# Kernel optimization log

Measured on AMD Instinct MI355X. Metric: run time of the kernel, lower is better.

## Reference

```python
import jax, jax.numpy as jnp
import numpy as np

N, E, H, D, F_IN = 50000, 400000, 2, 128, 5
EPS = 1e-5  # BatchNorm eps

def _bn(x, gamma, beta, rm, rv):
    # eval-mode BatchNorm1d using running stats
    return (x - rm) * jax.lax.rsqrt(rv + EPS) * gamma + beta

def setup_inputs() -> dict:
    key = jax.random.key(0)
    ks = jax.random.split(key, 24)
    r = lambda i, shape, s=1.0: jax.random.normal(ks[i], shape, jnp.float32) * s
    u = lambda i, shape: jax.random.uniform(ks[i], shape, jnp.float32)
    return {
        "h": r(0, (N, F_IN)),
        "edge_index": jax.random.randint(ks[1], (2, E), 0, N),
        "edge_weight": r(2, (E, 1)),
        # BatchNorm1d(5)
        "gamma1": 1.0 + r(3, (F_IN,), 0.1), "beta1": r(4, (F_IN,), 0.1),
        "rm1": r(5, (F_IN,), 0.1), "rv1": 0.5 + u(6, (F_IN,)),
        # GATv2Conv params (lin_l, lin_r with bias; lin_edge no bias; att; out bias)
        "Wl": r(7, (F_IN, H * D), 0.2), "bl": r(8, (H * D,), 0.1),
        "Wr": r(9, (F_IN, H * D), 0.2), "br": r(10, (H * D,), 0.1),
        "We": r(11, (1, H * D), 0.2),
        "att": r(12, (H, D), 0.2),
        "bias_gat": r(13, (D,), 0.1),
        # fc1 + BatchNorm1d(128)
        "W1": r(14, (D, D), 0.08), "b1": r(15, (D,), 0.1),
        "gamma2": 1.0 + r(16, (D,), 0.1), "beta2": r(17, (D,), 0.1),
        "rm2": r(18, (D,), 0.1), "rv2": 0.5 + u(19, (D,)),
        # fc2
        "W2": r(20, (D, F_IN), 0.08), "b2": r(21, (F_IN,), 0.1),
    }

def reference(h, edge_index, edge_weight, gamma1, beta1, rm1, rv1,
              Wl, bl, Wr, br, We, att, bias_gat,
              W1, b1, gamma2, beta2, rm2, rv2, W2, b2):
    src, dst = edge_index[0], edge_index[1]
    h = _bn(h, gamma1, beta1, rm1, rv1)
    xl = (h @ Wl + bl).reshape(N, H, D)   # source transform (messages)
    xr = (h @ Wr + br).reshape(N, H, D)   # destination transform
    e = (edge_weight @ We).reshape(E, H, D)
    # GATv2: score = att . leaky_relu(x_j + x_i + edge_emb), slope 0.2
    z = jax.nn.leaky_relu(xl[src] + xr[dst] + e, 0.2)          # [E,H,D]
    logits = jnp.einsum('ehd,hd->eh', z, att)                   # [E,H]
    # segment softmax over edges sharing a destination node
    mx = jax.ops.segment_max(logits, dst, num_segments=N)       # [N,H]
    ex = jnp.exp(logits - mx[dst])
    den = jax.ops.segment_sum(ex, dst, num_segments=N)
    alpha = ex / (den[dst] + 1e-16)                             # [E,H]
    msg = xl[src] * alpha[:, :, None]                           # [E,H,D]
    ssum = jax.ops.segment_sum(msg, dst, num_segments=N)        # [N,H,D]
    cnt = jax.ops.segment_sum(jnp.ones((E,), jnp.float32), dst, num_segments=N)
    out = ssum / jnp.maximum(cnt, 1.0)[:, None, None]           # aggr='mean'
    out = out.mean(axis=1) + bias_gat                           # concat=False -> head mean
    out = out @ W1 + b1
    out = _bn(out, gamma2, beta2, rm2, rv2)
    out = jax.nn.leaky_relu(out, 0.01)
    # dropout is identity in eval mode
    out = out @ W2 + b2                                         # [N,5]
    return out
```

## Files before the change

kernel.cpp:

```cpp
#include <hip/hip_runtime.h>

#define N_NODES 50000
#define N_EDGES 400000
#define F_INP 5
#define HD 256
#define BN_EPS 1e-5f

typedef short v8s __attribute__((ext_vector_type(8)));
typedef float v4f __attribute__((ext_vector_type(4)));
typedef unsigned v4u __attribute__((ext_vector_type(4)));

#define OFF_HBN  0
#define OFF_ACC  400000
#define OFF_BPK  1200000
#define OFF_WF   1202048
#define OFF_W2P  1204096

__device__ __forceinline__ unsigned short f2bf(float f) {
    unsigned u = __float_as_uint(f);
    return (unsigned short)((u + 0x7FFFu + ((u >> 16) & 1u)) >> 16);
}
__device__ __forceinline__ unsigned pk2(float a, float b) {
    return (unsigned)f2bf(a) | ((unsigned)f2bf(b) << 16);
}

__device__ __forceinline__ float wcat(int k, int c, const float* Wl, const float* Wr,
                                      const float* We, const float* bl, const float* br) {
    if (k < 5)   return Wl[k * HD + c];
    if (k < 10)  return Wr[(k - 5) * HD + c];
    if (k == 10) return We[c];
    return bl[c] + br[c];
}

__global__ void k_prep(const float* __restrict__ h, const float* __restrict__ g1,
                       const float* __restrict__ be1, const float* __restrict__ rm1,
                       const float* __restrict__ rv1,
                       const float* __restrict__ Wl, const float* __restrict__ bl,
                       const float* __restrict__ Wr, const float* __restrict__ br,
                       const float* __restrict__ We, const float* __restrict__ att,
                       float* __restrict__ hbn8, float* __restrict__ acc,
                       unsigned* __restrict__ Bpk) {
    int i = blockIdx.x * blockDim.x + threadIdx.x;
    if (i < N_NODES * 16) acc[i] = 0.f;
    if (i < N_NODES * 8) {
        int f = i & 7, n = i >> 3;
        float v = 0.f;
        if (f < F_INP) {
            float x = h[n * F_INP + f];
            v = (x - rm1[f]) * rsqrtf(rv1[f] + BN_EPS) * g1[f] + be1[f];
        }
        hbn8[i] = v;
    }
    if (i < 1024) {
        int t = i >> 6, l = i & 63;
        int g = l >> 4, c = t * 16 + (l & 15);
        unsigned d0 = 0, d1 = 0;
        if (g < 3) {
            int kb = 4 * g;
            d0 = pk2(wcat(kb + 0, c, Wl, Wr, We, bl, br),
                     wcat(kb + 1, c, Wl, Wr, We, bl, br));
            d1 = pk2(wcat(kb + 2, c, Wl, Wr, We, bl, br),
                     wcat(kb + 3, c, Wl, Wr, We, bl, br));
        }
        Bpk[(t * 64 + l) * 2 + 0] = d0;
        Bpk[(t * 64 + l) * 2 + 1] = d1;
    }
}

__global__ void k_pack2(const float* __restrict__ Wl, const float* __restrict__ bl,
                        const float* __restrict__ bias_gat,
                        const float* __restrict__ W1, const float* __restrict__ b1,
                        const float* __restrict__ g2, const float* __restrict__ be2,
                        const float* __restrict__ rm2, const float* __restrict__ rv2,
                        const float* __restrict__ W2,
                        float* __restrict__ Wf, float* __restrict__ W2p) {
    int k = blockIdx.x;
    int c = threadIdx.x;
    const float* base = (k == 0) ? bl
                      : (k == 1) ? bl + 128
                      : (k < 7)  ? Wl + (k - 2) * HD
                      : (k < 12) ? Wl + (k - 7) * HD + 128
                                 : bias_gat;
    float sum = 0.f;
#pragma unroll 8
    for (int d = 0; d < 128; ++d) sum += base[d] * W1[d * 128 + c];
    if (k == 12) sum += b1[c];
    Wf[c * 16 + k] = sum;
    if (k == 0) {
        float sc = g2[c] * rsqrtf(rv2[c] + BN_EPS);
        Wf[c * 16 + 13] = sc;
        Wf[c * 16 + 14] = be2[c] - rm2[c] * sc;
        Wf[c * 16 + 15] = 0.f;
#pragma unroll
        for (int f = 0; f < 8; ++f)
            W2p[c * 8 + f] = (f < 5) ? W2[c * 5 + f] : 0.f;
    }
}

__launch_bounds__(256)
__global__ void k_edge(const float* __restrict__ hbn8, const int* __restrict__ ei,
                       const float* __restrict__ ew, const unsigned* __restrict__ Bpk,
                       const float* __restrict__ att, float* __restrict__ acc) {
    int lane = threadIdx.x & 63;
    int wv = threadIdx.x >> 6;
    int g = lane >> 4, e16 = lane & 15;

    v8s B[16];
    float AT[16];
#pragma unroll
    for (int t = 0; t < 16; ++t) {
        unsigned d0 = Bpk[(t * 64 + lane) * 2 + 0];
        unsigned d1 = Bpk[(t * 64 + lane) * 2 + 1];
        v4u u = {d0, d1, 0u, 0u};
        B[t] = __builtin_bit_cast(v8s, u);
        AT[t] = att[t * 16 + e16];
    }

    int wid = blockIdx.x * 4 + wv;
    int nw = gridDim.x * 4;
    const int NT = N_EDGES / 16;

    int q13 = lane / 13;
    int j13 = lane - q13 * 13;
    bool sc_act = lane < 52;
    int kk = (j13 < 6) ? j13 - 1 : j13 - 7;
    int kc = min(max(kk, 0), 4);

    float x0 = 0, x1 = 0, x2 = 0, x3 = 0, x4 = 0,
          x5 = 0, x6 = 0, x7 = 0, x8 = 0, x9 = 0, x10 = 0;
    int dst_reg = 0;
    if (wid < NT && lane < 16) {
        int e = wid * 16 + lane;
        int src = ei[e];
        dst_reg = ei[N_EDGES + e];
        x10 = ew[e];
        float4 s4 = *(const float4*)&hbn8[src * 8];
        x0 = s4.x; x1 = s4.y; x2 = s4.z; x3 = s4.w;
        x4 = hbn8[src * 8 + 4];
        float4 d4 = *(const float4*)&hbn8[dst_reg * 8];
        x5 = d4.x; x6 = d4.y; x7 = d4.z; x8 = d4.w;
        x9 = hbn8[dst_reg * 8 + 4];
    }

    for (int tile = wid; tile < NT; tile += nw) {
        float b0 = __shfl(x0, e16), b1 = __shfl(x1, e16), b2 = __shfl(x2, e16),
              b3 = __shfl(x3, e16), b4 = __shfl(x4, e16), b5 = __shfl(x5, e16),
              b6 = __shfl(x6, e16), b7 = __shfl(x7, e16), b8 = __shfl(x8, e16),
              b9 = __shfl(x9, e16), b10 = __shfl(x10, e16);
        int dst_b = __shfl(dst_reg, e16);

        float a0 = (g == 0) ? b0 : (g == 1) ? b4 : b8;
        float a1 = (g == 0) ? b1 : (g == 1) ? b5 : b9;
        float a2 = (g == 0) ? b2 : (g == 1) ? b6 : b10;
        float a3 = (g == 0) ? b3 : (g == 1) ? b7 : 1.0f;
        unsigned ua0 = (g < 3) ? pk2(a0, a1) : 0u;
        unsigned ua1 = (g < 3) ? pk2(a2, a3) : 0u;
        v4u uav = {ua0, ua1, 0u, 0u};
        v8s A = __builtin_bit_cast(v8s, uav);

        int tn = tile + nw;
        if (tn < NT && lane < 16) {
            int e = tn * 16 + lane;
            int src = ei[e];
            dst_reg = ei[N_EDGES + e];
            x10 = ew[e];
            float4 s4 = *(const float4*)&hbn8[src * 8];
            x0 = s4.x; x1 = s4.y; x2 = s4.z; x3 = s4.w;
            x4 = hbn8[src * 8 + 4];
            float4 d4 = *(const float4*)&hbn8[dst_reg * 8];
            x5 = d4.x; x6 = d4.y; x7 = d4.z; x8 = d4.w;
            x9 = hbn8[dst_reg * 8 + 4];
        }

        float p00 = 0.f, p01 = 0.f, p02 = 0.f, p03 = 0.f;
        float p10 = 0.f, p11 = 0.f, p12 = 0.f, p13v = 0.f;
        v4f zero = {0.f, 0.f, 0.f, 0.f};
#pragma unroll
        for (int t = 0; t < 8; ++t) {
            v4f c = __builtin_amdgcn_mfma_f32_16x16x32_bf16(A, B[t], zero, 0, 0, 0);
            p00 += AT[t] * fmaf(0.66666667f, fabsf(c[0]), c[0]);
            p01 += AT[t] * fmaf(0.66666667f, fabsf(c[1]), c[1]);
            p02 += AT[t] * fmaf(0.66666667f, fabsf(c[2]), c[2]);
            p03 += AT[t] * fmaf(0.66666667f, fabsf(c[3]), c[3]);
        }
#pragma unroll
        for (int t = 8; t < 16; ++t) {
            v4f c = __builtin_amdgcn_mfma_f32_16x16x32_bf16(A, B[t], zero, 0, 0, 0);
            p10 += AT[t] * fmaf(0.66666667f, fabsf(c[0]), c[0]);
            p11 += AT[t] * fmaf(0.66666667f, fabsf(c[1]), c[1]);
            p12 += AT[t] * fmaf(0.66666667f, fabsf(c[2]), c[2]);
            p13v += AT[t] * fmaf(0.66666667f, fabsf(c[3]), c[3]);
        }
#pragma unroll
        for (int m = 1; m <= 8; m <<= 1) {
            p00 += __shfl_xor(p00, m); p01 += __shfl_xor(p01, m);
            p02 += __shfl_xor(p02, m); p03 += __shfl_xor(p03, m);
            p10 += __shfl_xor(p10, m); p11 += __shfl_xor(p11, m);
            p12 += __shfl_xor(p12, m); p13v += __shfl_xor(p13v, m);
        }
        float e00 = __expf(0.6f * p00), e01 = __expf(0.6f * p01);
        float e02 = __expf(0.6f * p02), e03 = __expf(0.6f * p03);
        float e10 = __expf(0.6f * p10), e11 = __expf(0.6f * p11);
        float e12 = __expf(0.6f * p12), e13 = __expf(0.6f * p13v);
        float tA0 = (lane & 1) ? e01 : e00;
        float tA1 = (lane & 1) ? e03 : e02;
        float exA = (lane & 2) ? tA1 : tA0;
        float tB0 = (lane & 1) ? e11 : e10;
        float tB1 = (lane & 1) ? e13 : e12;
        float exB = (lane & 2) ? tB1 : tB0;

        if (sc_act) {
#pragma unroll
            for (int it = 0; it < 4; ++it) {
                int es = it * 4 + q13;
                float h0 = __shfl(b0, es), h1 = __shfl(b1, es), h2 = __shfl(b2, es),
                      h3 = __shfl(b3, es), h4 = __shfl(b4, es);
                int de = __shfl(dst_b, es);
                float xh0 = __shfl(exA, it * 16 + q13);
                float xh1 = __shfl(exB, it * 16 + q13);
                float hsel = h0;
                hsel = (kc == 1) ? h1 : hsel;
                hsel = (kc == 2) ? h2 : hsel;
                hsel = (kc == 3) ? h3 : hsel;
                hsel = (kc == 4) ? h4 : hsel;
                float base = (j13 < 6) ? xh0 : xh1;
                float v = base * hsel;
                v = (j13 == 0) ? xh0 : v;
                v = (j13 == 6) ? xh1 : v;
                v = (j13 == 12) ? 1.0f : v;
                atomicAdd(&acc[de * 16 + j13], v);
            }
        }
    }
}

__launch_bounds__(256)
__global__ void k_mlp(const float* __restrict__ acc, const float* __restrict__ Wf,
                      const float* __restrict__ W2p, const float* __restrict__ b2,
                      float* __restrict__ out) {
    int n = blockIdx.x * blockDim.x + threadIdx.x;
    if (n >= N_NODES) return;
    const float* ar = acc + (size_t)n * 16;
    float4 A0 = *(const float4*)(ar + 0);
    float4 A1 = *(const float4*)(ar + 4);
    float4 A2 = *(const float4*)(ar + 8);
    float cnt = ar[12];
    float r0 = 1.f / (A0.x + 1e-16f);
    float r1 = 1.f / (A1.z + 1e-16f);
    float scale = 0.5f / fmaxf(cnt, 1.f);
    float s0 = scale * r0, s1 = scale * r1;
    float m0 = A0.x * s0, m1 = A1.z * s1;
    float m2 = A0.y * s0, m3 = A0.z * s0, m4 = A0.w * s0, m5 = A1.x * s0, m6 = A1.y * s0;
    float m7 = A1.w * s1, m8 = A2.x * s1, m9 = A2.y * s1, m10 = A2.z * s1, m11 = A2.w * s1;

    float o0 = 0.f, o1 = 0.f, o2 = 0.f, o3 = 0.f, o4 = 0.f;
#pragma unroll 4
    for (int c = 0; c < 128; ++c) {
        const float* wr = &Wf[c * 16];
        float a = wr[12];
        a += m0 * wr[0] + m1 * wr[1] + m2 * wr[2] + m3 * wr[3];
        a += m4 * wr[4] + m5 * wr[5] + m6 * wr[6] + m7 * wr[7];
        a += m8 * wr[8] + m9 * wr[9] + m10 * wr[10] + m11 * wr[11];
        a = fmaf(a, wr[13], wr[14]);
        a = fmaxf(a, 0.01f * a);
        const float* w2 = &W2p[c * 8];
        o0 = fmaf(a, w2[0], o0);
        o1 = fmaf(a, w2[1], o1);
        o2 = fmaf(a, w2[2], o2);
        o3 = fmaf(a, w2[3], o3);
        o4 = fmaf(a, w2[4], o4);
    }
    float* op = out + (size_t)n * 5;
    op[0] = o0 + b2[0];
    op[1] = o1 + b2[1];
    op[2] = o2 + b2[2];
    op[3] = o3 + b2[3];
    op[4] = o4 + b2[4];
}

extern "C" void kernel_launch(void* const* d_in, const int* in_sizes, int n_in,
                              void* d_out, int out_size, void* d_ws, size_t ws_size,
                              hipStream_t stream) {
    const float* h    = (const float*)d_in[0];
    const int*   ei   = (const int*)d_in[1];
    const float* ew   = (const float*)d_in[2];
    const float* g1   = (const float*)d_in[3];
    const float* be1  = (const float*)d_in[4];
    const float* rm1  = (const float*)d_in[5];
    const float* rv1  = (const float*)d_in[6];
    const float* Wl   = (const float*)d_in[7];
    const float* bl   = (const float*)d_in[8];
    const float* Wr   = (const float*)d_in[9];
    const float* br   = (const float*)d_in[10];
    const float* We   = (const float*)d_in[11];
    const float* att  = (const float*)d_in[12];
    const float* bias_gat = (const float*)d_in[13];
    const float* W1   = (const float*)d_in[14];
    const float* b1   = (const float*)d_in[15];
    const float* g2   = (const float*)d_in[16];
    const float* be2  = (const float*)d_in[17];
    const float* rm2  = (const float*)d_in[18];
    const float* rv2  = (const float*)d_in[19];
    const float* W2   = (const float*)d_in[20];
    const float* b2   = (const float*)d_in[21];

    float* ws  = (float*)d_ws;
    float* hbn = ws + OFF_HBN;
    float* acc = ws + OFF_ACC;
    unsigned* Bpk = (unsigned*)(ws + OFF_BPK);
    float* Wf  = ws + OFF_WF;
    float* W2p = ws + OFF_W2P;

    k_prep<<<(N_NODES * 16 + 255) / 256, 256, 0, stream>>>(
        h, g1, be1, rm1, rv1, Wl, bl, Wr, br, We, att, hbn, acc, Bpk);
    k_pack2<<<13, 128, 0, stream>>>(Wl, bl, bias_gat, W1, b1, g2, be2, rm2, rv2, W2,
                                    Wf, W2p);
    k_edge<<<1024, 256, 0, stream>>>(hbn, ei, ew, Bpk, att, acc);
    k_mlp<<<(N_NODES + 255) / 256, 256, 0, stream>>>(acc, Wf, W2p, b2, (float*)d_out);
}
```

Before: 87.45 us.

## Merge prep kernels, load edge data per group, use DPP reductions

Folds the weight-packing kernel into the prep kernel as extra blocks, removing one launch. The edge kernel stops software-prefetching the next tile through 16 lanes plus broadcast shuffles; each 16-lane group now loads its edge data directly and re-reads src/dst/features from global memory for the scatter phase. The cross-lane reductions switch from shuffles to DPP row rotates, and the edge grid grows from 1024 to 1280 blocks. This trades shuffle traffic for extra, mostly cached, redundant global loads and drops the explicit load/compute overlap.

After: 87.57 us. Within noise of the previous version (+0.1%).

```diff
diff --git a/kernel.cpp b/kernel.cpp
--- a/kernel.cpp
+++ b/kernel.cpp
@@ -15,6 +15,11 @@
 #define OFF_BPK  1200000
 #define OFF_WF   1202048
 #define OFF_W2P  1204096
+
+#define PREP_BLOCKS 3125
+
+#define DPP_ROR_F(x, n) \
+    __int_as_float(__builtin_amdgcn_update_dpp(0, __float_as_int(x), 0x120 | (n), 0xF, 0xF, false))
 
 __device__ __forceinline__ unsigned short f2bf(float f) {
     unsigned u = __float_as_uint(f);
@@ -38,44 +43,45 @@
                        const float* __restrict__ Wl, const float* __restrict__ bl,
                        const float* __restrict__ Wr, const float* __restrict__ br,
                        const float* __restrict__ We, const float* __restrict__ att,
+                       const float* __restrict__ bias_gat,
+                       const float* __restrict__ W1, const float* __restrict__ b1,
+                       const float* __restrict__ g2, const float* __restrict__ be2,
+                       const float* __restrict__ rm2, const float* __restrict__ rv2,
+                       const float* __restrict__ W2,
                        float* __restrict__ hbn8, float* __restrict__ acc,
-                       unsigned* __restrict__ Bpk) {
-    int i = blockIdx.x * blockDim.x + threadIdx.x;
-    if (i < N_NODES * 16) acc[i] = 0.f;
-    if (i < N_NODES * 8) {
-        int f = i & 7, n = i >> 3;
-        float v = 0.f;
-        if (f < F_INP) {
-            float x = h[n * F_INP + f];
-            v = (x - rm1[f]) * rsqrtf(rv1[f] + BN_EPS) * g1[f] + be1[f];
-        }
-        hbn8[i] = v;
-    }
-    if (i < 1024) {
-        int t = i >> 6, l = i & 63;
-        int g = l >> 4, c = t * 16 + (l & 15);
-        unsigned d0 = 0, d1 = 0;
-        if (g < 3) {
-            int kb = 4 * g;
-            d0 = pk2(wcat(kb + 0, c, Wl, Wr, We, bl, br),
-                     wcat(kb + 1, c, Wl, Wr, We, bl, br));
-            d1 = pk2(wcat(kb + 2, c, Wl, Wr, We, bl, br),
-                     wcat(kb + 3, c, Wl, Wr, We, bl, br));
-        }
-        Bpk[(t * 64 + l) * 2 + 0] = d0;
-        Bpk[(t * 64 + l) * 2 + 1] = d1;
-    }
-}
-
-__global__ void k_pack2(const float* __restrict__ Wl, const float* __restrict__ bl,
-                        const float* __restrict__ bias_gat,
-                        const float* __restrict__ W1, const float* __restrict__ b1,
-                        const float* __restrict__ g2, const float* __restrict__ be2,
-                        const float* __restrict__ rm2, const float* __restrict__ rv2,
-                        const float* __restrict__ W2,
-                        float* __restrict__ Wf, float* __restrict__ W2p) {
-    int k = blockIdx.x;
+                       unsigned* __restrict__ Bpk,
+                       float* __restrict__ Wf, float* __restrict__ W2p) {
+    if (blockIdx.x < PREP_BLOCKS) {
+        int i = blockIdx.x * blockDim.x + threadIdx.x;
+        if (i < N_NODES * 16) acc[i] = 0.f;
+        if (i < N_NODES * 8) {
+            int f = i & 7, n = i >> 3;
+            float v = 0.f;
+            if (f < F_INP) {
+                float x = h[n * F_INP + f];
+                v = (x - rm1[f]) * rsqrtf(rv1[f] + BN_EPS) * g1[f] + be1[f];
+            }
+            hbn8[i] = v;
+        }
+        if (i < 1024) {
+            int t = i >> 6, l = i & 63;
+            int g = l >> 4, c = t * 16 + (l & 15);
+            unsigned d0 = 0, d1 = 0;
+            if (g < 3) {
+                int kb = 4 * g;
+                d0 = pk2(wcat(kb + 0, c, Wl, Wr, We, bl, br),
+                         wcat(kb + 1, c, Wl, Wr, We, bl, br));
+                d1 = pk2(wcat(kb + 2, c, Wl, Wr, We, bl, br),
+                         wcat(kb + 3, c, Wl, Wr, We, bl, br));
+            }
+            Bpk[(t * 64 + l) * 2 + 0] = d0;
+            Bpk[(t * 64 + l) * 2 + 1] = d1;
+        }
+        return;
+    }
+    int k = blockIdx.x - PREP_BLOCKS;
     int c = threadIdx.x;
+    if (c >= 128) return;
     const float* base = (k == 0) ? bl
                       : (k == 1) ? bl + 128
                       : (k < 7)  ? Wl + (k - 2) * HD
@@ -109,9 +115,8 @@
     float AT[16];
 #pragma unroll
     for (int t = 0; t < 16; ++t) {
-        unsigned d0 = Bpk[(t * 64 + lane) * 2 + 0];
-        unsigned d1 = Bpk[(t * 64 + lane) * 2 + 1];
-        v4u u = {d0, d1, 0u, 0u};
+        uint2 d = *(const uint2*)&Bpk[(t * 64 + lane) * 2];
+        v4u u = {d.x, d.y, 0u, 0u};
         B[t] = __builtin_bit_cast(v8s, u);
         AT[t] = att[t * 16 + e16];
     }
@@ -120,57 +125,29 @@
     int nw = gridDim.x * 4;
     const int NT = N_EDGES / 16;
 
-    int q13 = lane / 13;
-    int j13 = lane - q13 * 13;
-    bool sc_act = lane < 52;
-    int kk = (j13 < 6) ? j13 - 1 : j13 - 7;
+    int j16 = e16;
+    bool sact = j16 < 13;
+    int kk = (j16 < 6) ? j16 - 1 : j16 - 7;
     int kc = min(max(kk, 0), 4);
 
-    float x0 = 0, x1 = 0, x2 = 0, x3 = 0, x4 = 0,
-          x5 = 0, x6 = 0, x7 = 0, x8 = 0, x9 = 0, x10 = 0;
-    int dst_reg = 0;
-    if (wid < NT && lane < 16) {
-        int e = wid * 16 + lane;
+    for (int tile = wid; tile < NT; tile += nw) {
+        int e = tile * 16 + e16;
         int src = ei[e];
-        dst_reg = ei[N_EDGES + e];
-        x10 = ew[e];
+        int dst = ei[N_EDGES + e];
+        float w = ew[e];
         float4 s4 = *(const float4*)&hbn8[src * 8];
-        x0 = s4.x; x1 = s4.y; x2 = s4.z; x3 = s4.w;
-        x4 = hbn8[src * 8 + 4];
-        float4 d4 = *(const float4*)&hbn8[dst_reg * 8];
-        x5 = d4.x; x6 = d4.y; x7 = d4.z; x8 = d4.w;
-        x9 = hbn8[dst_reg * 8 + 4];
-    }
-
-    for (int tile = wid; tile < NT; tile += nw) {
-        float b0 = __shfl(x0, e16), b1 = __shfl(x1, e16), b2 = __shfl(x2, e16),
-              b3 = __shfl(x3, e16), b4 = __shfl(x4, e16), b5 = __shfl(x5, e16),
-              b6 = __shfl(x6, e16), b7 = __shfl(x7, e16), b8 = __shfl(x8, e16),
-              b9 = __shfl(x9, e16), b10 = __shfl(x10, e16);
-        int dst_b = __shfl(dst_reg, e16);
-
-        float a0 = (g == 0) ? b0 : (g == 1) ? b4 : b8;
-        float a1 = (g == 0) ? b1 : (g == 1) ? b5 : b9;
-        float a2 = (g == 0) ? b2 : (g == 1) ? b6 : b10;
-        float a3 = (g == 0) ? b3 : (g == 1) ? b7 : 1.0f;
+        float hs4 = hbn8[src * 8 + 4];
+        float4 d4 = *(const float4*)&hbn8[dst * 8];
+        float hd4 = hbn8[dst * 8 + 4];
+
+        float a0 = (g == 0) ? s4.x : (g == 1) ? hs4  : d4.w;
+        float a1 = (g == 0) ? s4.y : (g == 1) ? d4.x : hd4;
+        float a2 = (g == 0) ? s4.z : (g == 1) ? d4.y : w;
+        float a3 = (g == 0) ? s4.w : (g == 1) ? d4.z : 1.0f;
         unsigned ua0 = (g < 3) ? pk2(a0, a1) : 0u;
         unsigned ua1 = (g < 3) ? pk2(a2, a3) : 0u;
         v4u uav = {ua0, ua1, 0u, 0u};
         v8s A = __builtin_bit_cast(v8s, uav);
-
-        int tn = tile + nw;
-        if (tn < NT && lane < 16) {
-            int e = tn * 16 + lane;
-            int src = ei[e];
-            dst_reg = ei[N_EDGES + e];
-            x10 = ew[e];
-            float4 s4 = *(const float4*)&hbn8[src * 8];
-            x0 = s4.x; x1 = s4.y; x2 = s4.z; x3 = s4.w;
-            x4 = hbn8[src * 8 + 4];
-            float4 d4 = *(const float4*)&hbn8[dst_reg * 8];
-            x5 = d4.x; x6 = d4.y; x7 = d4.z; x8 = d4.w;
-            x9 = hbn8[dst_reg * 8 + 4];
-        }
 
         float p00 = 0.f, p01 = 0.f, p02 = 0.f, p03 = 0.f;
         float p10 = 0.f, p11 = 0.f, p12 = 0.f, p13v = 0.f;
@@ -192,43 +169,49 @@
             p13v += AT[t] * fmaf(0.66666667f, fabsf(c[3]), c[3]);
         }
 #pragma unroll
-        for (int m = 1; m <= 8; m <<= 1) {
-            p00 += __shfl_xor(p00, m); p01 += __shfl_xor(p01, m);
-            p02 += __shfl_xor(p02, m); p03 += __shfl_xor(p03, m);
-            p10 += __shfl_xor(p10, m); p11 += __shfl_xor(p11, m);
-            p12 += __shfl_xor(p12, m); p13v += __shfl_xor(p13v, m);
+        for (int st = 1; st <= 8; st <<= 1) {
+            if (st == 1) {
+                p00 += DPP_ROR_F(p00, 1); p01 += DPP_ROR_F(p01, 1);
+                p02 += DPP_ROR_F(p02, 1); p03 += DPP_ROR_F(p03, 1);
+                p10 += DPP_ROR_F(p10, 1); p11 += DPP_ROR_F(p11, 1);
+                p12 += DPP_ROR_F(p12, 1); p13v += DPP_ROR_F(p13v, 1);
+            } else if (st == 2) {
+                p00 += DPP_ROR_F(p00, 2); p01 += DPP_ROR_F(p01, 2);
+                p02 += DPP_ROR_F(p02, 2); p03 += DPP_ROR_F(p03, 2);
+                p10 += DPP_ROR_F(p10, 2); p11 += DPP_ROR_F(p11, 2);
+                p12 += DPP_ROR_F(p12, 2); p13v += DPP_ROR_F(p13v, 2);
+            } else if (st == 4) {
+                p00 += DPP_ROR_F(p00, 4); p01 += DPP_ROR_F(p01, 4);
+                p02 += DPP_ROR_F(p02, 4); p03 += DPP_ROR_F(p03, 4);
+                p10 += DPP_ROR_F(p10, 4); p11 += DPP_ROR_F(p11, 4);
+                p12 += DPP_ROR_F(p12, 4); p13v += DPP_ROR_F(p13v, 4);
+            } else {
+                p00 += DPP_ROR_F(p00, 8); p01 += DPP_ROR_F(p01, 8);
+                p02 += DPP_ROR_F(p02, 8); p03 += DPP_ROR_F(p03, 8);
+                p10 += DPP_ROR_F(p10, 8); p11 += DPP_ROR_F(p11, 8);
+                p12 += DPP_ROR_F(p12, 8); p13v += DPP_ROR_F(p13v, 8);
+            }
         }
         float e00 = __expf(0.6f * p00), e01 = __expf(0.6f * p01);
         float e02 = __expf(0.6f * p02), e03 = __expf(0.6f * p03);
         float e10 = __expf(0.6f * p10), e11 = __expf(0.6f * p11);
         float e12 = __expf(0.6f * p12), e13 = __expf(0.6f * p13v);
-        float tA0 = (lane & 1) ? e01 : e00;
-        float tA1 = (lane & 1) ? e03 : e02;
-        float exA = (lane & 2) ? tA1 : tA0;
-        float tB0 = (lane & 1) ? e11 : e10;
-        float tB1 = (lane & 1) ? e13 : e12;
-        float exB = (lane & 2) ? tB1 : tB0;
-
-        if (sc_act) {
+
+        if (sact) {
 #pragma unroll
             for (int it = 0; it < 4; ++it) {
-                int es = it * 4 + q13;
-                float h0 = __shfl(b0, es), h1 = __shfl(b1, es), h2 = __shfl(b2, es),
-                      h3 = __shfl(b3, es), h4 = __shfl(b4, es);
-                int de = __shfl(dst_b, es);
-                float xh0 = __shfl(exA, it * 16 + q13);
-                float xh1 = __shfl(exB, it * 16 + q13);
-                float hsel = h0;
-                hsel = (kc == 1) ? h1 : hsel;
-                hsel = (kc == 2) ? h2 : hsel;
-                hsel = (kc == 3) ? h3 : hsel;
-                hsel = (kc == 4) ? h4 : hsel;
-                float base = (j13 < 6) ? xh0 : xh1;
+                int eg = tile * 16 + 4 * g + it;
+                int srcg = ei[eg];
+                int deg = ei[N_EDGES + eg];
+                float hsel = hbn8[srcg * 8 + kc];
+                float ex0 = (it == 0) ? e00 : (it == 1) ? e01 : (it == 2) ? e02 : e03;
+                float ex1 = (it == 0) ? e10 : (it == 1) ? e11 : (it == 2) ? e12 : e13;
+                float base = (j16 < 6) ? ex0 : ex1;
                 float v = base * hsel;
-                v = (j13 == 0) ? xh0 : v;
-                v = (j13 == 6) ? xh1 : v;
-                v = (j13 == 12) ? 1.0f : v;
-                atomicAdd(&acc[de * 16 + j13], v);
+                v = (j16 == 0) ? ex0 : v;
+                v = (j16 == 6) ? ex1 : v;
+                v = (j16 == 12) ? 1.0f : v;
+                atomicAdd(&acc[deg * 16 + j16], v);
             }
         }
     }
@@ -311,10 +294,9 @@
     float* Wf  = ws + OFF_WF;
     float* W2p = ws + OFF_W2P;
 
-    k_prep<<<(N_NODES * 16 + 255) / 256, 256, 0, stream>>>(
-        h, g1, be1, rm1, rv1, Wl, bl, Wr, br, We, att, hbn, acc, Bpk);
-    k_pack2<<<13, 128, 0, stream>>>(Wl, bl, bias_gat, W1, b1, g2, be2, rm2, rv2, W2,
-                                    Wf, W2p);
-    k_edge<<<1024, 256, 0, stream>>>(hbn, ei, ew, Bpk, att, acc);
+    k_prep<<<PREP_BLOCKS + 13, 256, 0, stream>>>(
+        h, g1, be1, rm1, rv1, Wl, bl, Wr, br, We, att, bias_gat,
+        W1, b1, g2, be2, rm2, rv2, W2, hbn, acc, Bpk, Wf, W2p);
+    k_edge<<<1280, 256, 0, stream>>>(hbn, ei, ew, Bpk, att, acc);
     k_mlp<<<(N_NODES + 255) / 256, 256, 0, stream>>>(acc, Wf, W2p, b2, (float*)d_out);
 }
```
